# Optimization experiments

Measured on AMD Instinct MI355X. Metric: run time of the kernel, lower is better.

## Reference

```python
import jax, jax.numpy as jnp
import numpy as np

EPS = 1e-08


def setup_inputs() -> dict:
    key = jax.random.key(0)
    ks = jax.random.split(key, 9)
    B, T, H, W = 128, 32, 32, 32
    Z = 128
    d = {}
    d['x_seq'] = jax.random.normal(ks[0], (B, T, H, W), dtype=jnp.float32)
    # encoder MLP: 1024 -> 256 -> 128 (kaiming-ish scale)
    d['We1'] = jax.random.normal(ks[1], (H * W, 256), dtype=jnp.float32) * (2.0 / (H * W)) ** 0.5
    d['be1'] = jnp.zeros((256,), jnp.float32)
    d['We2'] = jax.random.normal(ks[2], (256, Z), dtype=jnp.float32) * (2.0 / 256) ** 0.5
    d['be2'] = jnp.zeros((Z,), jnp.float32)
    # context norm params
    d['gamma'] = jnp.ones((Z,), jnp.float32)
    d['beta'] = jnp.zeros((Z,), jnp.float32)
    # g_theta: (128+1)*2=258 -> 512 -> 256
    d['Wg1'] = jax.random.normal(ks[3], (258, 512), dtype=jnp.float32) * (2.0 / 258) ** 0.5
    d['bg1'] = jnp.zeros((512,), jnp.float32)
    d['Wg2'] = jax.random.normal(ks[4], (512, 256), dtype=jnp.float32) * (2.0 / 512) ** 0.5
    d['bg2'] = jnp.zeros((256,), jnp.float32)
    # f_phi: 256 -> 256 -> y_dim=4
    d['Wf'] = jax.random.normal(ks[5], (256, 256), dtype=jnp.float32) * (2.0 / 256) ** 0.5
    d['bf'] = jnp.zeros((256,), jnp.float32)
    d['Wy'] = jax.random.normal(ks[6], (256, 4), dtype=jnp.float32) * (1.0 / 256) ** 0.5
    d['by'] = jnp.zeros((4,), jnp.float32)
    return d


def reference(x_seq, We1, be1, We2, be2, gamma, beta, Wg1, bg1, Wg2, bg2, Wf, bf, Wy, by):
    B, T, H, W = x_seq.shape
    # Encoder (MLP stand-in), vectorized over the sequence dim
    x = x_seq.reshape(B, T, H * W)
    h = jax.nn.relu(jnp.einsum('btd,dk->btk', x, We1) + be1)
    z = jnp.einsum('btk,kz->btz', h, We2) + be2          # [B,T,128]
    # Context norm over the sequence dim (torch .var() is unbiased, ddof=1)
    mu = z.mean(axis=1, keepdims=True)
    sigma = jnp.sqrt(z.var(axis=1, keepdims=True, ddof=1) + EPS)
    z = (z - mu) / sigma * gamma + beta
    # Append temporal tag
    tag = jnp.broadcast_to(jnp.arange(T, dtype=z.dtype)[None, :, None], (B, T, 1))
    z = jnp.concatenate([z, tag], axis=2)                # [B,T,129]
    # Relation network over all T^2 ordered pairs, batched as one GEMM.
    # g_hidden = relu([z_i, z_j] @ Wg1 + bg1); split Wg1 to avoid materializing the concat.
    Wg1_a, Wg1_b = Wg1[:129], Wg1[129:]
    gi = jnp.einsum('bic,ch->bih', z, Wg1_a)             # [B,T,512]
    gj = jnp.einsum('bjc,ch->bjh', z, Wg1_b)             # [B,T,512]
    g_hidden = jax.nn.relu(gi[:, :, None, :] + gj[:, None, :, :] + bg1)  # [B,T,T,512]
    g_out = jax.nn.relu(jnp.einsum('bijh,hg->bijg', g_hidden, Wg2) + bg2)
    all_g = g_out.sum(axis=(1, 2))                       # [B,256]
    f_hidden = jax.nn.relu(all_g @ Wf + bf)
    y_pred_linear = f_hidden @ Wy + by                   # [B,4]
    y_pred = jnp.argmax(y_pred_linear, axis=1)
    return (y_pred_linear, y_pred)
```

## Files before the change

### kernel.cpp

```cpp
#include <hip/hip_runtime.h>
#include <hip/hip_bf16.h>

#define EPS 1e-8f

typedef __attribute__((ext_vector_type(8))) short short8;
typedef __attribute__((ext_vector_type(4))) float f32x4;

__device__ __forceinline__ unsigned short f2bf(float f) {
  union { float f; unsigned u; } v; v.f = f;
  unsigned r = v.u + 0x7fffu + ((v.u >> 16) & 1u);
  return (unsigned short)(r >> 16);
}
__device__ __forceinline__ float bf2f(unsigned short b) {
  union { unsigned u; float f; } v; v.u = ((unsigned)b) << 16;
  return v.f;
}
__device__ __forceinline__ unsigned pack_bf2(float lo, float hi) {
  unsigned r;
  asm("v_cvt_pk_bf16_f32 %0, %1, %2" : "=v"(r) : "v"(lo), "v"(hi));
  return r;
}

__global__ __launch_bounds__(256) void k0_prep(const float* __restrict__ We1,
                                               const float* __restrict__ We2,
                                               const float* __restrict__ Wg1,
                                               const float* __restrict__ Wg2,
                                               const float* __restrict__ Wf,
                                               unsigned short* __restrict__ We1T,
                                               unsigned short* __restrict__ We2T,
                                               unsigned short* __restrict__ Wg1T,
                                               unsigned short* __restrict__ Wg2T,
                                               unsigned short* __restrict__ WfT) {
  int idx = blockIdx.x * 256 + threadIdx.x;
  if (idx < 262144) {
    int n = idx >> 10, k = idx & 1023;
    We1T[idx] = f2bf(We1[k * 256 + n]);
  } else if (idx < 294912) {
    int e = idx - 262144;
    int n = e >> 8, k = e & 255;
    We2T[e] = f2bf(We2[k * 128 + n]);
  } else if (idx < 458752) {
    int e = idx - 294912;
    int n = e / 160, c = e % 160;
    float v = 0.f;
    if (c < 129) v = (n < 512) ? Wg1[c * 512 + n] : Wg1[(129 + c) * 512 + (n - 512)];
    Wg1T[e] = f2bf(v);
  } else if (idx < 589824) {
    int e = idx - 458752;
    int n = e >> 9, k = e & 511;
    Wg2T[e] = f2bf(Wg2[k * 256 + n]);
  } else {
    int e = idx - 589824;
    int n = e >> 8, k = e & 255;
    WfT[e] = f2bf(Wf[k * 256 + n]);
  }
}

__global__ __launch_bounds__(512, 2) void k1(const float* __restrict__ x,
                                             const unsigned short* __restrict__ We1T,
                                             const float* __restrict__ be1,
                                             unsigned short* __restrict__ h_bf) {
  __shared__ unsigned char As[2][8192];
  int tid = threadIdx.x, lane = tid & 63, w = tid >> 6;
  int m0 = blockIdx.x * 16;
  int srow = tid >> 5, skk = (tid & 31) * 8;
  int cb = w * 32;
  int row = lane & 15, kg = (lane >> 4) * 8;

  f32x4 acc[2] = {{0,0,0,0},{0,0,0,0}};

  auto stage = [&](int kc, int buf) {
    const float* src = x + (size_t)(m0 + srow) * 1024 + kc * 256 + skk;
    float4 a = *reinterpret_cast<const float4*>(src);
    float4 b = *reinterpret_cast<const float4*>(src + 4);
    uint4 pv;
    pv.x = pack_bf2(a.x, a.y); pv.y = pack_bf2(a.z, a.w);
    pv.z = pack_bf2(b.x, b.y); pv.w = pack_bf2(b.z, b.w);
    int addr = (srow * 512 + skk * 2) ^ ((srow & 7) << 4);
    *reinterpret_cast<uint4*>(&As[buf][addr]) = pv;
  };

  stage(0, 0);
  __syncthreads();
  for (int kc = 0; kc < 4; ++kc) {
    if (kc < 3) stage(kc + 1, (kc + 1) & 1);
    short8 breg[2][8];
#pragma unroll
    for (int cf = 0; cf < 2; ++cf)
#pragma unroll
      for (int ks = 0; ks < 8; ++ks)
        breg[cf][ks] = *reinterpret_cast<const short8*>(
            We1T + (size_t)(cb + cf * 16 + row) * 1024 + kc * 256 + ks * 32 + kg);
    const unsigned char* hc = &As[kc & 1][0];
#pragma unroll
    for (int ks = 0; ks < 8; ++ks) {
      int aoff = (row * 512 + ks * 64 + kg * 2) ^ ((row & 7) << 4);
      short8 af = *reinterpret_cast<const short8*>(hc + aoff);
      acc[0] = __builtin_amdgcn_mfma_f32_16x16x32_bf16(af, breg[0][ks], acc[0], 0, 0, 0);
      acc[1] = __builtin_amdgcn_mfma_f32_16x16x32_bf16(af, breg[1][ks], acc[1], 0, 0, 0);
    }
    __syncthreads();
  }
#pragma unroll
  for (int cf = 0; cf < 2; ++cf) {
    int col = cb + cf * 16 + row;
    float bias = be1[col];
#pragma unroll
    for (int r = 0; r < 4; ++r) {
      int orow = m0 + (lane >> 4) * 4 + r;
      h_bf[(size_t)orow * 256 + col] = f2bf(fmaxf(acc[cf][r] + bias, 0.f));
    }
  }
}

__global__ __launch_bounds__(256) void k2a(const unsigned short* __restrict__ h_bf,
                                           const unsigned short* __restrict__ We2T,
                                           const float* __restrict__ be2,
                                           const float* __restrict__ gamma,
                                           const float* __restrict__ beta,
                                           unsigned short* __restrict__ zc) {
  __shared__ unsigned char zcs[16384];
  __shared__ float zb[32][132];
  int b = blockIdx.x, tid = threadIdx.x, lane = tid & 63, w = tid >> 6;
  int row = lane & 15, kg = (lane >> 4) * 8;

  {
    int srow = tid >> 3, skk = (tid & 7) * 32;
#pragma unroll
    for (int q = 0; q < 4; ++q) {
      short8 v = *reinterpret_cast<const short8*>(
          h_bf + (size_t)(b * 32 + srow) * 256 + skk + q * 8);
      int addr = (srow * 512 + (skk + q * 8) * 2) ^ ((srow & 7) << 4);
      *reinterpret_cast<short8*>(&zcs[addr]) = v;
    }
  }
  short8 breg1[2][8];
#pragma unroll
  for (int cf = 0; cf < 2; ++cf)
#pragma unroll
    for (int ks = 0; ks < 8; ++ks)
      breg1[cf][ks] = *reinterpret_cast<const short8*>(
          We2T + (size_t)(w * 32 + cf * 16 + row) * 256 + ks * 32 + kg);
  __syncthreads();

  {
    f32x4 acc[2][2] = {{{0,0,0,0},{0,0,0,0}},{{0,0,0,0},{0,0,0,0}}};
#pragma unroll
    for (int ks = 0; ks < 8; ++ks) {
      int a0off = (row * 512 + ks * 64 + kg * 2) ^ ((row & 7) << 4);
      int a1off = ((16 + row) * 512 + ks * 64 + kg * 2) ^ ((row & 7) << 4);
      short8 a0 = *reinterpret_cast<const short8*>(&zcs[a0off]);
      short8 a1 = *reinterpret_cast<const short8*>(&zcs[a1off]);
#pragma unroll
      for (int cf = 0; cf < 2; ++cf) {
        acc[0][cf] = __builtin_amdgcn_mfma_f32_16x16x32_bf16(a0, breg1[cf][ks], acc[0][cf], 0, 0, 0);
        acc[1][cf] = __builtin_amdgcn_mfma_f32_16x16x32_bf16(a1, breg1[cf][ks], acc[1][cf], 0, 0, 0);
      }
    }
#pragma unroll
    for (int rf = 0; rf < 2; ++rf)
#pragma unroll
      for (int cf = 0; cf < 2; ++cf) {
        int col = w * 32 + cf * 16 + row;
        float bias = be2[col];
#pragma unroll
        for (int r = 0; r < 4; ++r)
          zb[rf * 16 + (lane >> 4) * 4 + r][col] = acc[rf][cf][r] + bias;
      }
  }
  __syncthreads();

  if (tid < 128) {
    float s = 0.f, s2 = 0.f;
#pragma unroll 4
    for (int t = 0; t < 32; ++t) { float v = zb[t][tid]; s += v; s2 += v * v; }
    float mu = s * (1.f / 32.f);
    float var = (s2 - 32.f * mu * mu) * (1.f / 31.f);
    float rs = 1.f / sqrtf(fmaxf(var, 0.f) + EPS);
    float g = gamma[tid], be = beta[tid];
#pragma unroll 4
    for (int t = 0; t < 32; ++t)
      zc[(size_t)(b * 32 + t) * 160 + tid] = f2bf((zb[t][tid] - mu) * rs * g + be);
  } else if (tid < 160) {
    for (int t = 0; t < 32; ++t)
      zc[(size_t)(b * 32 + t) * 160 + tid] = (tid == 128) ? f2bf((float)t) : 0;
  }
}

__global__ __launch_bounds__(512, 4) void k2b(const unsigned short* __restrict__ zc,
                                              const unsigned short* __restrict__ Wg1T,
                                              const float* __restrict__ bg1,
                                              unsigned short* __restrict__ g_all) {
  __shared__ unsigned char As[16384];
  int m0 = (blockIdx.x >> 2) * 32;
  int n0 = (blockIdx.x & 3) * 256;
  int tid = threadIdx.x, lane = tid & 63, w = tid >> 6;
  int row = lane & 15, kg = (lane >> 4) * 8;
  int c0 = n0 + w * 32;

  for (int ch = tid; ch < 640; ch += 512) {
    int r = ch / 20, c16 = ch % 20;
    short8 v = *reinterpret_cast<const short8*>(zc + (size_t)(m0 + r) * 160 + c16 * 8);
    int addr = (r * 512 + c16 * 16) ^ ((r & 7) << 4);
    *reinterpret_cast<short8*>(&As[addr]) = v;
  }
  short8 breg[2][5];
#pragma unroll
  for (int cf = 0; cf < 2; ++cf)
#pragma unroll
    for (int ks = 0; ks < 5; ++ks)
      breg[cf][ks] = *reinterpret_cast<const short8*>(
          Wg1T + (size_t)(c0 + cf * 16 + row) * 160 + ks * 32 + kg);
  __syncthreads();

  f32x4 acc[2][2] = {{{0,0,0,0},{0,0,0,0}},{{0,0,0,0},{0,0,0,0}}};
#pragma unroll
  for (int ks = 0; ks < 5; ++ks) {
    int a0off = (row * 512 + ks * 64 + kg * 2) ^ ((row & 7) << 4);
    int a1off = ((16 + row) * 512 + ks * 64 + kg * 2) ^ ((row & 7) << 4);
    short8 a0 = *reinterpret_cast<const short8*>(&As[a0off]);
    short8 a1 = *reinterpret_cast<const short8*>(&As[a1off]);
#pragma unroll
    for (int cf = 0; cf < 2; ++cf) {
      acc[0][cf] = __builtin_amdgcn_mfma_f32_16x16x32_bf16(a0, breg[cf][ks], acc[0][cf], 0, 0, 0);
      acc[1][cf] = __builtin_amdgcn_mfma_f32_16x16x32_bf16(a1, breg[cf][ks], acc[1][cf], 0, 0, 0);
    }
  }
#pragma unroll
  for (int cf = 0; cf < 2; ++cf) {
    int n = c0 + cf * 16 + row;
    float bias = (n < 512) ? bg1[n] : 0.f;
#pragma unroll
    for (int rf = 0; rf < 2; ++rf)
#pragma unroll
      for (int r = 0; r < 4; ++r) {
        int mrow = m0 + rf * 16 + (lane >> 4) * 4 + r;
        g_all[((size_t)mrow << 10) + n] = f2bf(acc[rf][cf][r] + bias);
      }
  }
}

__global__ __launch_bounds__(512, 2) void k3(const unsigned short* __restrict__ g_all,
                                             const unsigned short* __restrict__ Wg2T,
                                             const float* __restrict__ bg2,
                                             float* __restrict__ all_gp) {
  __shared__ unsigned char ldsH[2][2][32768];
  int b = blockIdx.x >> 1, hi = blockIdx.x & 1;
  int ii0 = hi * 16;
  int tid = threadIdx.x, lane = tid & 63, w = tid >> 6;
  int row = lane & 15, kg = (lane >> 4) * 8;
  int cb = w * 32;
  int p = tid >> 4, kslot = tid & 15;

  short8 breg[2][16];
#pragma unroll
  for (int cf = 0; cf < 2; ++cf)
#pragma unroll
    for (int ks = 0; ks < 16; ++ks)
      breg[cf][ks] = *reinterpret_cast<const short8*>(
          Wg2T + (size_t)(cb + cf * 16 + row) * 512 + ks * 32 + kg);

  short8 gjr[4];
  {
    const unsigned short* gjp = g_all + ((size_t)(b * 32 + p) << 10) + 512 + kslot * 8;
#pragma unroll
    for (int q = 0; q < 4; ++q)
      gjr[q] = *reinterpret_cast<const short8*>(gjp + q * 128);
  }
  float biasv[2] = { bg2[cb + row], bg2[cb + 16 + row] };
  float accsum[2] = { 0.f, 0.f };

  short8 gv[4];
  auto hload = [&](int ii) {
    const unsigned short* gi = g_all + ((size_t)(b * 32 + ii) << 10) + kslot * 8;
#pragma unroll
    for (int q = 0; q < 4; ++q)
      gv[q] = *reinterpret_cast<const short8*>(gi + q * 128);
  };
  auto hstore = [&](int buf, int sub) {
    unsigned char* hb = &ldsH[buf][sub][0] + p * 1024;
#pragma unroll
    for (int q = 0; q < 4; ++q) {
      float f0 = fmaxf(bf2f((unsigned short)gv[q][0]) + bf2f((unsigned short)gjr[q][0]), 0.f);
      float f1 = fmaxf(bf2f((unsigned short)gv[q][1]) + bf2f((unsigned short)gjr[q][1]), 0.f);
      float f2 = fmaxf(bf2f((unsigned short)gv[q][2]) + bf2f((unsigned short)gjr[q][2]), 0.f);
      float f3 = fmaxf(bf2f((unsigned short)gv[q][3]) + bf2f((unsigned short)gjr[q][3]), 0.f);
      float f4 = fmaxf(bf2f((unsigned short)gv[q][4]) + bf2f((unsigned short)gjr[q][4]), 0.f);
      float f5 = fmaxf(bf2f((unsigned short)gv[q][5]) + bf2f((unsigned short)gjr[q][5]), 0.f);
      float f6 = fmaxf(bf2f((unsigned short)gv[q][6]) + bf2f((unsigned short)gjr[q][6]), 0.f);
      float f7 = fmaxf(bf2f((unsigned short)gv[q][7]) + bf2f((unsigned short)gjr[q][7]), 0.f);
      uint4 pv;
      pv.x = pack_bf2(f0, f1); pv.y = pack_bf2(f2, f3);
      pv.z = pack_bf2(f4, f5); pv.w = pack_bf2(f6, f7);
      int addr = (kslot * 16 + q * 256) ^ ((p & 7) << 4);
      *reinterpret_cast<uint4*>(hb + addr) = pv;
    }
  };
  auto aread = [&](const unsigned char* hc, int r, int ks) {
    return *reinterpret_cast<const short8*>(
        hc + ((r * 1024 + ks * 64 + kg * 2) ^ ((r & 7) << 4)));
  };
  auto subtile = [&](int buf, int sub) {
    const unsigned char* hc = &ldsH[buf][sub][0];
    f32x4 acc[2][2] = {{{0,0,0,0},{0,0,0,0}},{{0,0,0,0},{0,0,0,0}}};
    short8 a0 = aread(hc, row, 0);
    short8 a1 = aread(hc, 16 + row, 0);
#pragma unroll
    for (int ks = 0; ks < 16; ++ks) {
      short8 c0v = a0, c1v = a1;
      if (ks < 15) {
        a0 = aread(hc, row, ks + 1);
        a1 = aread(hc, 16 + row, ks + 1);
      }
      __builtin_amdgcn_s_setprio(1);
      acc[0][0] = __builtin_amdgcn_mfma_f32_16x16x32_bf16(c0v, breg[0][ks], acc[0][0], 0, 0, 0);
      acc[0][1] = __builtin_amdgcn_mfma_f32_16x16x32_bf16(c0v, breg[1][ks], acc[0][1], 0, 0, 0);
      acc[1][0] = __builtin_amdgcn_mfma_f32_16x16x32_bf16(c1v, breg[0][ks], acc[1][0], 0, 0, 0);
      acc[1][1] = __builtin_amdgcn_mfma_f32_16x16x32_bf16(c1v, breg[1][ks], acc[1][1], 0, 0, 0);
      __builtin_amdgcn_s_setprio(0);
    }
#pragma unroll
    for (int cf = 0; cf < 2; ++cf)
#pragma unroll
      for (int rf = 0; rf < 2; ++rf)
#pragma unroll
        for (int r = 0; r < 4; ++r)
          accsum[cf] += fmaxf(acc[rf][cf][r] + biasv[cf], 0.f);
  };

  hload(ii0);     hstore(0, 0);
  hload(ii0 + 1); hstore(0, 1);
  __syncthreads();

  for (int it = 0; it < 8; ++it) {
    int cur = it & 1, nxt = cur ^ 1;
    bool more = (it < 7);
    if (more) hload(ii0 + 2 * it + 2);
    subtile(cur, 0);
    if (more) {
      hstore(nxt, 0);
      hload(ii0 + 2 * it + 3);
    }
    subtile(cur, 1);
    if (more) hstore(nxt, 1);
    __syncthreads();
  }

#pragma unroll
  for (int cf = 0; cf < 2; ++cf) {
    accsum[cf] += __shfl_xor(accsum[cf], 16, 64);
    accsum[cf] += __shfl_xor(accsum[cf], 32, 64);
  }
  if ((lane >> 4) == 0) {
#pragma unroll
    for (int cf = 0; cf < 2; ++cf)
      all_gp[(size_t)(hi * 128 + b) * 256 + cb + cf * 16 + lane] = accsum[cf];
  }
}

__global__ __launch_bounds__(512) void k4(const float* __restrict__ all_gp,
                                          const unsigned short* __restrict__ WfT,
                                          const float* __restrict__ bfv,
                                          const float* __restrict__ Wy,
                                          const float* __restrict__ by,
                                          float* __restrict__ out) {
  __shared__ unsigned char As[8192];
  __shared__ float fh[16][264];
  __shared__ float wys[1024];
  __shared__ float yvs[16][4];
  int tid = threadIdx.x, lane = tid & 63, w = tid >> 6;
  int row = lane & 15, kg = (lane >> 4) * 8;
  int m0 = blockIdx.x * 16;

  {
    int r = tid >> 5, c8 = (tid & 31) * 8;
    float s[8];
#pragma unroll
    for (int e = 0; e < 8; ++e) s[e] = 0.f;
#pragma unroll
    for (int q = 0; q < 2; ++q) {
      const float* p0 = all_gp + (size_t)(q * 128 + m0 + r) * 256 + c8;
      float4 a0 = *reinterpret_cast<const float4*>(p0);
      float4 a1 = *reinterpret_cast<const float4*>(p0 + 4);
      s[0] += a0.x; s[1] += a0.y; s[2] += a0.z; s[3] += a0.w;
      s[4] += a1.x; s[5] += a1.y; s[6] += a1.z; s[7] += a1.w;
    }
    uint4 pv;
    pv.x = pack_bf2(s[0], s[1]); pv.y = pack_bf2(s[2], s[3]);
    pv.z = pack_bf2(s[4], s[5]); pv.w = pack_bf2(s[6], s[7]);
    int addr = (r * 512 + c8 * 2) ^ ((r & 7) << 4);
    *reinterpret_cast<uint4*>(&As[addr]) = pv;
  }
  wys[tid] = Wy[tid];
  wys[tid + 512] = Wy[tid + 512];
  short8 breg[2][8];
#pragma unroll
  for (int cf = 0; cf < 2; ++cf)
#pragma unroll
    for (int ks = 0; ks < 8; ++ks)
      breg[cf][ks] = *reinterpret_cast<const short8*>(
          WfT + (size_t)(w * 32 + cf * 16 + row) * 256 + ks * 32 + kg);
  __syncthreads();

  f32x4 acc[2] = {{0,0,0,0},{0,0,0,0}};
#pragma unroll
  for (int ks = 0; ks < 8; ++ks) {
    int aoff = (row * 512 + ks * 64 + kg * 2) ^ ((row & 7) << 4);
    short8 af = *reinterpret_cast<const short8*>(&As[aoff]);
    acc[0] = __builtin_amdgcn_mfma_f32_16x16x32_bf16(af, breg[0][ks], acc[0], 0, 0, 0);
    acc[1] = __builtin_amdgcn_mfma_f32_16x16x32_bf16(af, breg[1][ks], acc[1], 0, 0, 0);
  }
#pragma unroll
  for (int cf = 0; cf < 2; ++cf) {
    int col = w * 32 + cf * 16 + row;
    float bias = bfv[col];
#pragma unroll
    for (int r = 0; r < 4; ++r)
      fh[(lane >> 4) * 4 + r][col] = fmaxf(acc[cf][r] + bias, 0.f);
  }
  __syncthreads();

  if (tid < 64) {
    int r = tid >> 2, o = tid & 3;
    float y = by[o];
#pragma unroll 4
    for (int k = 0; k < 256; ++k) y += fh[r][k] * wys[k * 4 + o];
    yvs[r][o] = y;
    out[(m0 + r) * 4 + o] = y;
  }
  __syncthreads();
  if (tid < 16) {
    int am = 0;
    float best = yvs[tid][0];
#pragma unroll
    for (int o = 1; o < 4; ++o)
      if (yvs[tid][o] > best) { best = yvs[tid][o]; am = o; }
    out[512 + m0 + tid] = (float)am;
  }
}

extern "C" void kernel_launch(void* const* d_in, const int* in_sizes, int n_in,
                              void* d_out, int out_size, void* d_ws, size_t ws_size,
                              hipStream_t stream) {
  const float* x     = (const float*)d_in[0];
  const float* We1   = (const float*)d_in[1];
  const float* be1   = (const float*)d_in[2];
  const float* We2   = (const float*)d_in[3];
  const float* be2   = (const float*)d_in[4];
  const float* gamma = (const float*)d_in[5];
  const float* beta  = (const float*)d_in[6];
  const float* Wg1   = (const float*)d_in[7];
  const float* bg1   = (const float*)d_in[8];
  const float* Wg2   = (const float*)d_in[9];
  const float* bg2   = (const float*)d_in[10];
  const float* Wf    = (const float*)d_in[11];
  const float* bff   = (const float*)d_in[12];
  const float* Wy    = (const float*)d_in[13];
  const float* by    = (const float*)d_in[14];

  char* ws = (char*)d_ws;
  unsigned short* h_bf  = (unsigned short*)(ws + 0);
  unsigned short* g_all = (unsigned short*)(ws + 2097152);
  unsigned short* We1T  = (unsigned short*)(ws + 10485760);
  unsigned short* We2T  = (unsigned short*)(ws + 11010048);
  unsigned short* Wg1T  = (unsigned short*)(ws + 11075584);
  unsigned short* Wg2T  = (unsigned short*)(ws + 11403264);
  float*          all_gp= (float*)(ws + 11665408);
  unsigned short* WfT   = (unsigned short*)(ws + 11927552);
  unsigned short* zc    = (unsigned short*)(ws + 12058624);
  float*          out   = (float*)d_out;

  k0_prep<<<2560, 256, 0, stream>>>(We1, We2, Wg1, Wg2, Wf, We1T, We2T, Wg1T, Wg2T, WfT);
  k1<<<256, 512, 0, stream>>>(x, We1T, be1, h_bf);
  k2a<<<128, 256, 0, stream>>>(h_bf, We2T, be2, gamma, beta, zc);
  k2b<<<512, 512, 0, stream>>>(zc, Wg1T, bg1, g_all);
  k3<<<256, 512, 0, stream>>>(g_all, Wg2T, bg2, all_gp);
  k4<<<8, 512, 0, stream>>>(all_gp, WfT, bff, Wy, by, out);
}
```

Baseline: 95.99 us.

## Build relation hidden fragments in registers instead of staging through LDS

The k3 relation kernel stops materialising the relu(gi+gj) hidden tile in double-buffered LDS between barriers. It now preloads the block's gi rows as fp32 and all gj rows as swizzled bf16 into LDS once, then builds the MFMA A-fragments directly in registers inside the K loop. This removes the per-subtile store/sync round trip. In exchange, every wave redundantly recomputes the add/relu/pack for its fragments, which increases VALU work interleaved with the MFMAs and adds LDS reads of fp32 gi per k-step.

```diff
diff --git a/kernel.cpp b/kernel.cpp
--- a/kernel.cpp
+++ b/kernel.cpp
@@ -19,6 +19,12 @@
   unsigned r;
   asm("v_cvt_pk_bf16_f32 %0, %1, %2" : "=v"(r) : "v"(lo), "v"(hi));
   return r;
+}
+__device__ __forceinline__ float ulo(unsigned u) {
+  union { unsigned u; float f; } v; v.u = u << 16; return v.f;
+}
+__device__ __forceinline__ float uhi(unsigned u) {
+  union { unsigned u; float f; } v; v.u = u & 0xffff0000u; return v.f;
 }
 
 __global__ __launch_bounds__(256) void k0_prep(const float* __restrict__ We1,
@@ -244,13 +250,13 @@
                                              const unsigned short* __restrict__ Wg2T,
                                              const float* __restrict__ bg2,
                                              float* __restrict__ all_gp) {
-  __shared__ unsigned char ldsH[2][2][32768];
+  __shared__ float giL[8192];
+  __shared__ unsigned char gjL[32768];
   int b = blockIdx.x >> 1, hi = blockIdx.x & 1;
   int ii0 = hi * 16;
   int tid = threadIdx.x, lane = tid & 63, w = tid >> 6;
-  int row = lane & 15, kg = (lane >> 4) * 8;
+  int r = lane & 15, q = lane >> 4;
   int cb = w * 32;
-  int p = tid >> 4, kslot = tid & 15;
 
   short8 breg[2][16];
 #pragma unroll
@@ -258,92 +264,84 @@
 #pragma unroll
     for (int ks = 0; ks < 16; ++ks)
       breg[cf][ks] = *reinterpret_cast<const short8*>(
-          Wg2T + (size_t)(cb + cf * 16 + row) * 512 + ks * 32 + kg);
-
-  short8 gjr[4];
-  {
-    const unsigned short* gjp = g_all + ((size_t)(b * 32 + p) << 10) + 512 + kslot * 8;
-#pragma unroll
-    for (int q = 0; q < 4; ++q)
-      gjr[q] = *reinterpret_cast<const short8*>(gjp + q * 128);
-  }
-  float biasv[2] = { bg2[cb + row], bg2[cb + 16 + row] };
+          Wg2T + (size_t)(cb + cf * 16 + r) * 512 + ks * 32 + q * 8);
+
+  for (int e = tid; e < 1024; e += 512) {
+    int rr = e >> 6, c8 = (e & 63) << 3;
+    short8 v = *reinterpret_cast<const short8*>(
+        g_all + ((size_t)(b * 32 + ii0 + rr) << 10) + c8);
+    float4 fa, fb;
+    fa.x = bf2f((unsigned short)v[0]); fa.y = bf2f((unsigned short)v[1]);
+    fa.z = bf2f((unsigned short)v[2]); fa.w = bf2f((unsigned short)v[3]);
+    fb.x = bf2f((unsigned short)v[4]); fb.y = bf2f((unsigned short)v[5]);
+    fb.z = bf2f((unsigned short)v[6]); fb.w = bf2f((unsigned short)v[7]);
+    *reinterpret_cast<float4*>(&giL[rr * 512 + c8]) = fa;
+    *reinterpret_cast<float4*>(&giL[rr * 512 + c8 + 4]) = fb;
+  }
+  for (int e = tid; e < 2048; e += 512) {
+    int rr = e >> 6, c8 = (e & 63) << 3;
+    short8 v = *reinterpret_cast<const short8*>(
+        g_all + ((size_t)(b * 32 + rr) << 10) + 512 + c8);
+    int addr = (rr * 1024 + c8 * 2) ^ ((rr & 7) << 4);
+    *reinterpret_cast<short8*>(&gjL[addr]) = v;
+  }
+  float biasv[2] = { bg2[cb + r], bg2[cb + 16 + r] };
   float accsum[2] = { 0.f, 0.f };
-
-  short8 gv[4];
-  auto hload = [&](int ii) {
-    const unsigned short* gi = g_all + ((size_t)(b * 32 + ii) << 10) + kslot * 8;
-#pragma unroll
-    for (int q = 0; q < 4; ++q)
-      gv[q] = *reinterpret_cast<const short8*>(gi + q * 128);
+  __syncthreads();
+
+  int swz = (r & 7) << 4;
+  int gjE = (r * 1024 + q * 16) ^ swz;
+  int gjO = (r * 1024 + 64 + q * 16) ^ swz;
+
+  auto mkfrag = [&](short8 gj, float4 a, float4 bb) {
+    uint4 u = *reinterpret_cast<uint4*>(&gj);
+    float f0 = fmaxf(a.x + ulo(u.x), 0.f);
+    float f1 = fmaxf(a.y + uhi(u.x), 0.f);
+    float f2 = fmaxf(a.z + ulo(u.y), 0.f);
+    float f3 = fmaxf(a.w + uhi(u.y), 0.f);
+    float f4 = fmaxf(bb.x + ulo(u.z), 0.f);
+    float f5 = fmaxf(bb.y + uhi(u.z), 0.f);
+    float f6 = fmaxf(bb.z + ulo(u.w), 0.f);
+    float f7 = fmaxf(bb.w + uhi(u.w), 0.f);
+    uint4 p;
+    p.x = pack_bf2(f0, f1); p.y = pack_bf2(f2, f3);
+    p.z = pack_bf2(f4, f5); p.w = pack_bf2(f6, f7);
+    return *reinterpret_cast<short8*>(&p);
   };
-  auto hstore = [&](int buf, int sub) {
-    unsigned char* hb = &ldsH[buf][sub][0] + p * 1024;
-#pragma unroll
-    for (int q = 0; q < 4; ++q) {
-      float f0 = fmaxf(bf2f((unsigned short)gv[q][0]) + bf2f((unsigned short)gjr[q][0]), 0.f);
-      float f1 = fmaxf(bf2f((unsigned short)gv[q][1]) + bf2f((unsigned short)gjr[q][1]), 0.f);
-      float f2 = fmaxf(bf2f((unsigned short)gv[q][2]) + bf2f((unsigned short)gjr[q][2]), 0.f);
-      float f3 = fmaxf(bf2f((unsigned short)gv[q][3]) + bf2f((unsigned short)gjr[q][3]), 0.f);
-      float f4 = fmaxf(bf2f((unsigned short)gv[q][4]) + bf2f((unsigned short)gjr[q][4]), 0.f);
-      float f5 = fmaxf(bf2f((unsigned short)gv[q][5]) + bf2f((unsigned short)gjr[q][5]), 0.f);
-      float f6 = fmaxf(bf2f((unsigned short)gv[q][6]) + bf2f((unsigned short)gjr[q][6]), 0.f);
-      float f7 = fmaxf(bf2f((unsigned short)gv[q][7]) + bf2f((unsigned short)gjr[q][7]), 0.f);
-      uint4 pv;
-      pv.x = pack_bf2(f0, f1); pv.y = pack_bf2(f2, f3);
-      pv.z = pack_bf2(f4, f5); pv.w = pack_bf2(f6, f7);
-      int addr = (kslot * 16 + q * 256) ^ ((p & 7) << 4);
-      *reinterpret_cast<uint4*>(hb + addr) = pv;
-    }
-  };
-  auto aread = [&](const unsigned char* hc, int r, int ks) {
-    return *reinterpret_cast<const short8*>(
-        hc + ((r * 1024 + ks * 64 + kg * 2) ^ ((r & 7) << 4)));
-  };
-  auto subtile = [&](int buf, int sub) {
-    const unsigned char* hc = &ldsH[buf][sub][0];
-    f32x4 acc[2][2] = {{{0,0,0,0},{0,0,0,0}},{{0,0,0,0},{0,0,0,0}}};
-    short8 a0 = aread(hc, row, 0);
-    short8 a1 = aread(hc, 16 + row, 0);
+
+#pragma unroll 1
+  for (int il = 0; il < 16; ++il) {
+    const float* gib = &giL[il * 512 + q * 8];
+    f32x4 acc00 = {0,0,0,0}, acc01 = {0,0,0,0}, acc10 = {0,0,0,0}, acc11 = {0,0,0,0};
+    short8 rgj0[2], rgj1[2];
+    float4 rgiA[2], rgiB[2];
+    rgj0[0] = *reinterpret_cast<const short8*>(gjL + gjE);
+    rgj1[0] = *reinterpret_cast<const short8*>(gjL + gjE + 16384);
+    rgiA[0] = *reinterpret_cast<const float4*>(gib);
+    rgiB[0] = *reinterpret_cast<const float4*>(gib + 4);
 #pragma unroll
     for (int ks = 0; ks < 16; ++ks) {
-      short8 c0v = a0, c1v = a1;
+      int cs = ks & 1, ns = cs ^ 1;
       if (ks < 15) {
-        a0 = aread(hc, row, ks + 1);
-        a1 = aread(hc, 16 + row, ks + 1);
+        int koff = ((ks + 1) >> 1) * 128;
+        int base = ((ks + 1) & 1) ? gjO : gjE;
+        rgj0[ns] = *reinterpret_cast<const short8*>(gjL + base + koff);
+        rgj1[ns] = *reinterpret_cast<const short8*>(gjL + base + koff + 16384);
+        rgiA[ns] = *reinterpret_cast<const float4*>(gib + (ks + 1) * 32);
+        rgiB[ns] = *reinterpret_cast<const float4*>(gib + (ks + 1) * 32 + 4);
       }
-      __builtin_amdgcn_s_setprio(1);
-      acc[0][0] = __builtin_amdgcn_mfma_f32_16x16x32_bf16(c0v, breg[0][ks], acc[0][0], 0, 0, 0);
-      acc[0][1] = __builtin_amdgcn_mfma_f32_16x16x32_bf16(c0v, breg[1][ks], acc[0][1], 0, 0, 0);
-      acc[1][0] = __builtin_amdgcn_mfma_f32_16x16x32_bf16(c1v, breg[0][ks], acc[1][0], 0, 0, 0);
-      acc[1][1] = __builtin_amdgcn_mfma_f32_16x16x32_bf16(c1v, breg[1][ks], acc[1][1], 0, 0, 0);
-      __builtin_amdgcn_s_setprio(0);
-    }
-#pragma unroll
-    for (int cf = 0; cf < 2; ++cf)
-#pragma unroll
-      for (int rf = 0; rf < 2; ++rf)
-#pragma unroll
-        for (int r = 0; r < 4; ++r)
-          accsum[cf] += fmaxf(acc[rf][cf][r] + biasv[cf], 0.f);
-  };
-
-  hload(ii0);     hstore(0, 0);
-  hload(ii0 + 1); hstore(0, 1);
-  __syncthreads();
-
-  for (int it = 0; it < 8; ++it) {
-    int cur = it & 1, nxt = cur ^ 1;
-    bool more = (it < 7);
-    if (more) hload(ii0 + 2 * it + 2);
-    subtile(cur, 0);
-    if (more) {
-      hstore(nxt, 0);
-      hload(ii0 + 2 * it + 3);
-    }
-    subtile(cur, 1);
-    if (more) hstore(nxt, 1);
-    __syncthreads();
+      short8 af0 = mkfrag(rgj0[cs], rgiA[cs], rgiB[cs]);
+      short8 af1 = mkfrag(rgj1[cs], rgiA[cs], rgiB[cs]);
+      acc00 = __builtin_amdgcn_mfma_f32_16x16x32_bf16(af0, breg[0][ks], acc00, 0, 0, 0);
+      acc01 = __builtin_amdgcn_mfma_f32_16x16x32_bf16(af0, breg[1][ks], acc01, 0, 0, 0);
+      acc10 = __builtin_amdgcn_mfma_f32_16x16x32_bf16(af1, breg[0][ks], acc10, 0, 0, 0);
+      acc11 = __builtin_amdgcn_mfma_f32_16x16x32_bf16(af1, breg[1][ks], acc11, 0, 0, 0);
+    }
+#pragma unroll
+    for (int e = 0; e < 4; ++e) {
+      accsum[0] += fmaxf(acc00[e] + biasv[0], 0.f) + fmaxf(acc10[e] + biasv[0], 0.f);
+      accsum[1] += fmaxf(acc01[e] + biasv[1], 0.f) + fmaxf(acc11[e] + biasv[1], 0.f);
+    }
   }
 
 #pragma unroll
```

Measured after the change: 117.6 us. 1.22x slower.
